# Performance work log

Hardware: AMD Instinct MI355X
Metric: run time of the kernel (lower is better)

The kernel has to match this reference:

```python
import jax, jax.numpy as jnp
import numpy as np

B = 128
N_ATOMS = 4096
NB, NA, NT = 4095, 4094, 4093
MAX_LEN = 5 * NT  # 20465, longest packed column (torsions)
EPS = 1e-8


def setup_inputs() -> dict:
    key = jax.random.key(0)
    ks = jax.random.split(key, 24)
    feats = jnp.zeros((B, MAX_LEN, 9), jnp.float32)
    # col 0: atom type ids
    atoms = jax.random.randint(ks[0], (B, N_ATOMS), 0, 6)
    # col 5: coords, flattened (N_ATOMS, 3)
    coords = jax.random.normal(ks[1], (B, N_ATOMS, 3), jnp.float32) * 5.0
    # col 6: bonds (i, j, type)
    bonds = jnp.stack([
        jax.random.randint(ks[2], (B, NB), 0, N_ATOMS),
        jax.random.randint(ks[3], (B, NB), 0, N_ATOMS),
        jax.random.randint(ks[4], (B, NB), 0, 15)], axis=-1)
    # col 7: angles (i, j, k, type)
    angles = jnp.stack([
        jax.random.randint(ks[5], (B, NA), 0, N_ATOMS),
        jax.random.randint(ks[6], (B, NA), 0, N_ATOMS),
        jax.random.randint(ks[7], (B, NA), 0, N_ATOMS),
        jax.random.randint(ks[8], (B, NA), 0, 13)], axis=-1)
    # col 8: torsions (i, j, k, l, type)
    tors = jnp.stack([
        jax.random.randint(ks[9], (B, NT), 0, N_ATOMS),
        jax.random.randint(ks[10], (B, NT), 0, N_ATOMS),
        jax.random.randint(ks[11], (B, NT), 0, N_ATOMS),
        jax.random.randint(ks[12], (B, NT), 0, N_ATOMS),
        jax.random.randint(ks[13], (B, NT), 0, 25)], axis=-1)
    feats = feats.at[:, :N_ATOMS, 0].set(atoms.astype(jnp.float32))
    feats = feats.at[:, :3 * N_ATOMS, 5].set(coords.reshape(B, -1))
    feats = feats.at[:, :3 * NB, 6].set(bonds.reshape(B, -1).astype(jnp.float32))
    feats = feats.at[:, :4 * NA, 7].set(angles.reshape(B, -1).astype(jnp.float32))
    feats = feats.at[:, :5 * NT, 8].set(tors.reshape(B, -1).astype(jnp.float32))
    lengths = jnp.tile(jnp.array(
        [[N_ATOMS, 0, 0, 0, 0, 3 * N_ATOMS, 3 * NB, 4 * NA, 5 * NT]],
        jnp.int32), (B, 1))
    bond_type = jnp.stack([jnp.ones(15), jax.random.uniform(ks[14], (15,), minval=1.0, maxval=2.0)], -1).astype(jnp.float32)
    angle_type = jnp.stack([jnp.ones(13), jax.random.uniform(ks[15], (13,), minval=1.0, maxval=3.0)], -1).astype(jnp.float32)
    tor_type = jnp.stack([jnp.ones(25), jax.random.uniform(ks[16], (25,), minval=0.0, maxval=3.14)], -1).astype(jnp.float32)
    multiplicity = jax.random.randint(ks[17], (25,), 1, 4)
    opt_pars = jax.random.uniform(ks[18], (47,), minval=0.5, maxval=1.5).astype(jnp.float32)
    return {"features": feats, "lengths": lengths, "bond_type": bond_type,
            "angle_type": angle_type, "tor_type": tor_type,
            "multiplicity": multiplicity, "opt_pars": opt_pars}


def _sample_energy(f, bond_type, angle_type, tor_type, multiplicity, opt_pars):
    coords = f[:3 * N_ATOMS, 5].reshape(-1, 3)                      # [N,3]
    bonds = f[:3 * NB, 6].astype(jnp.int32).reshape(-1, 3)          # [NB,3]
    angles = f[:4 * NA, 7].astype(jnp.int32).reshape(-1, 4)         # [NA,4]
    tors = f[:5 * NT, 8].astype(jnp.int32).reshape(-1, 5)           # [NT,5]

    # bonds: harmonic k*(r - r0)^2
    d = coords[bonds[:, 0]] - coords[bonds[:, 1]]
    r = jnp.sqrt(jnp.sum(d * d, -1) + EPS)
    pb = bond_type[bonds[:, 2]]
    e_bond = opt_pars[0] * jnp.sum(pb[:, 0] * (r - pb[:, 1]) ** 2)

    # angles: harmonic k*(theta - theta0)^2
    v1 = coords[angles[:, 0]] - coords[angles[:, 1]]
    v2 = coords[angles[:, 2]] - coords[angles[:, 1]]
    cosang = jnp.sum(v1 * v2, -1) / (
        jnp.sqrt(jnp.sum(v1 * v1, -1) + EPS) * jnp.sqrt(jnp.sum(v2 * v2, -1) + EPS))
    theta = jnp.arccos(jnp.clip(cosang, -1.0 + 1e-6, 1.0 - 1e-6))
    pa = angle_type[angles[:, 3]]
    e_ang = opt_pars[1] * jnp.sum(pa[:, 0] * (theta - pa[:, 1]) ** 2)

    # torsions: periodic k*(1 + cos(n*phi - delta))
    ci, cj, ck, cl = (coords[tors[:, m]] for m in range(4))
    b1, b2, b3 = cj - ci, ck - cj, cl - ck
    n1 = jnp.cross(b1, b2)
    n2 = jnp.cross(b2, b3)
    b2n = b2 / jnp.sqrt(jnp.sum(b2 * b2, -1, keepdims=True) + EPS)
    m1 = jnp.cross(n1, b2n)
    phi = jnp.arctan2(jnp.sum(m1 * n2, -1), jnp.sum(n1 * n2, -1))
    pt = tor_type[tors[:, 4]]
    n_mult = multiplicity[tors[:, 4]].astype(jnp.float32)
    e_tor = opt_pars[2] * jnp.sum(pt[:, 0] * (1.0 + jnp.cos(n_mult * phi - pt[:, 1])))

    return jnp.stack([e_bond, e_ang, e_tor])


def reference(features, lengths, bond_type, angle_type, tor_type, multiplicity, opt_pars):
    # lengths are uniform across batch (constants above); vmap over batch dim
    return jax.vmap(_sample_energy, in_axes=(0, None, None, None, None, None))(
        features, bond_type, angle_type, tor_type, multiplicity, opt_pars)
```

## Files before the change

### kernel.cpp

```cpp
#include <hip/hip_runtime.h>
#include <math.h>

#define BATCH   128
#define N_ATOMS 4096
#define NB      4095
#define NA      4094
#define NT      4093
#define MAX_LEN (5 * NT)
#define FSTRIDE ((size_t)MAX_LEN * 9)
#define EPSV    1e-8f
#define PARTS   6
#define THREADS 256

__global__ __launch_bounds__(THREADS) void
local_energy_kernel(const float* __restrict__ F,
                    const float* __restrict__ bond_type,
                    const float* __restrict__ angle_type,
                    const float* __restrict__ tor_type,
                    const int*   __restrict__ multiplicity,
                    const float* __restrict__ opt_pars,
                    float*       __restrict__ out)
{
    __shared__ float scx[N_ATOMS];
    __shared__ float scy[N_ATOMS];
    __shared__ float scz[N_ATOMS];
    __shared__ float sbt[30];
    __shared__ float sat[26];
    __shared__ float stt[50];
    __shared__ float smu[25];
    __shared__ float sred[12];

    const int b   = blockIdx.x;
    const int x   = b & 7;
    const int g   = b >> 3;
    const int s   = (g & 15) * 8 + x;
    const int p   = g >> 4;
    const int tid = threadIdx.x;
    const float* __restrict__ Fb = F + (size_t)s * FSTRIDE;

    if (tid < 30)                      sbt[tid]       = bond_type[tid];
    else if (tid >= 32 && tid < 58)    sat[tid - 32]  = angle_type[tid - 32];
    else if (tid >= 64 && tid < 114)   stt[tid - 64]  = tor_type[tid - 64];
    else if (tid >= 128 && tid < 153)  smu[tid - 128] = (float)multiplicity[tid - 128];

    for (int a = tid; a < N_ATOMS; a += THREADS) {
        const float* cp = Fb + 27 * a;
        float vx = cp[5];
        float vy = cp[14];
        float vz = cp[23];
        scx[a] = vx;
        scy[a] = vy;
        scz[a] = vz;
    }
    __syncthreads();

    float e_bond = 0.0f, e_ang = 0.0f, e_tor = 0.0f;

    {
        const int chunk = (NB + PARTS - 1) / PARTS;
        const int lo = p * chunk;
        const int hi = (lo + chunk < NB) ? (lo + chunk) : NB;
        for (int i = lo + tid; i < hi; i += THREADS) {
            const float* bp = Fb + 27 * i + 6;
            int a0 = (int)bp[0];
            int a1 = (int)bp[9];
            int bt = (int)bp[18];
            float dx = scx[a0] - scx[a1];
            float dy = scy[a0] - scy[a1];
            float dz = scz[a0] - scz[a1];
            float r  = sqrtf(dx*dx + dy*dy + dz*dz + EPSV);
            float k0 = sbt[bt * 2 + 0];
            float r0 = sbt[bt * 2 + 1];
            float t  = r - r0;
            e_bond += k0 * t * t;
        }
    }

    {
        const int chunk = (NA + PARTS - 1) / PARTS;
        const int lo = p * chunk;
        const int hi = (lo + chunk < NA) ? (lo + chunk) : NA;
        for (int i = lo + tid; i < hi; i += THREADS) {
            const float* ap = Fb + 36 * i + 7;
            int a0 = (int)ap[0];
            int a1 = (int)ap[9];
            int a2 = (int)ap[18];
            int at = (int)ap[27];
            float v1x = scx[a0] - scx[a1];
            float v1y = scy[a0] - scy[a1];
            float v1z = scz[a0] - scz[a1];
            float v2x = scx[a2] - scx[a1];
            float v2y = scy[a2] - scy[a1];
            float v2z = scz[a2] - scz[a1];
            float d12 = v1x*v2x + v1y*v2y + v1z*v2z;
            float n1  = sqrtf(v1x*v1x + v1y*v1y + v1z*v1z + EPSV);
            float n2  = sqrtf(v2x*v2x + v2y*v2y + v2z*v2z + EPSV);
            float cosang = d12 / (n1 * n2);
            cosang = fminf(fmaxf(cosang, -1.0f + 1e-6f), 1.0f - 1e-6f);
            float theta = acosf(cosang);
            float k0 = sat[at * 2 + 0];
            float t0 = sat[at * 2 + 1];
            float t  = theta - t0;
            e_ang += k0 * t * t;
        }
    }

    {
        const int chunk = (NT + PARTS - 1) / PARTS;
        const int lo = p * chunk;
        const int hi = (lo + chunk < NT) ? (lo + chunk) : NT;
        for (int i = lo + tid; i < hi; i += THREADS) {
            const float* tp = Fb + 45 * i + 8;
            int ai = (int)tp[0];
            int aj = (int)tp[9];
            int ak = (int)tp[18];
            int al = (int)tp[27];
            int tt = (int)tp[36];

            float cix = scx[ai], ciy = scy[ai], ciz = scz[ai];
            float cjx = scx[aj], cjy = scy[aj], cjz = scz[aj];
            float ckx = scx[ak], cky = scy[ak], ckz = scz[ak];
            float clx = scx[al], cly = scy[al], clz = scz[al];

            float b1x = cjx - cix, b1y = cjy - ciy, b1z = cjz - ciz;
            float b2x = ckx - cjx, b2y = cky - cjy, b2z = ckz - cjz;
            float b3x = clx - ckx, b3y = cly - cky, b3z = clz - ckz;

            float n1x = b1y*b2z - b1z*b2y;
            float n1y = b1z*b2x - b1x*b2z;
            float n1z = b1x*b2y - b1y*b2x;
            float n2x = b2y*b3z - b2z*b3y;
            float n2y = b2z*b3x - b2x*b3z;
            float n2z = b2x*b3y - b2y*b3x;

            float b2len = sqrtf(b2x*b2x + b2y*b2y + b2z*b2z + EPSV);
            float inv   = 1.0f / b2len;
            float bnx = b2x * inv, bny = b2y * inv, bnz = b2z * inv;

            float m1x = n1y*bnz - n1z*bny;
            float m1y = n1z*bnx - n1x*bnz;
            float m1z = n1x*bny - n1y*bnx;

            float sy = m1x*n2x + m1y*n2y + m1z*n2z;
            float sx = n1x*n2x + n1y*n2y + n1z*n2z;
            float phi = atan2f(sy, sx);

            float k0  = stt[tt * 2 + 0];
            float ph0 = stt[tt * 2 + 1];
            float nm  = smu[tt];
            e_tor += k0 * (1.0f + cosf(nm * phi - ph0));
        }
    }

    for (int off = 32; off > 0; off >>= 1) {
        e_bond += __shfl_down(e_bond, off);
        e_ang  += __shfl_down(e_ang,  off);
        e_tor  += __shfl_down(e_tor,  off);
    }
    const int wave = tid >> 6;
    const int lane = tid & 63;
    if (lane == 0) {
        sred[wave * 3 + 0] = e_bond;
        sred[wave * 3 + 1] = e_ang;
        sred[wave * 3 + 2] = e_tor;
    }
    __syncthreads();
    if (tid == 0) {
        float eb = 0.0f, ea = 0.0f, et = 0.0f;
        for (int w = 0; w < THREADS / 64; ++w) {
            eb += sred[w * 3 + 0];
            ea += sred[w * 3 + 1];
            et += sred[w * 3 + 2];
        }
        atomicAdd(&out[s * 3 + 0], opt_pars[0] * eb);
        atomicAdd(&out[s * 3 + 1], opt_pars[1] * ea);
        atomicAdd(&out[s * 3 + 2], opt_pars[2] * et);
    }
}

extern "C" void kernel_launch(void* const* d_in, const int* in_sizes, int n_in,
                              void* d_out, int out_size, void* d_ws, size_t ws_size,
                              hipStream_t stream) {
    const float* F            = (const float*)d_in[0];
    const float* bond_type    = (const float*)d_in[2];
    const float* angle_type   = (const float*)d_in[3];
    const float* tor_type     = (const float*)d_in[4];
    const int*   multiplicity = (const int*)  d_in[5];
    const float* opt_pars     = (const float*)d_in[6];
    float* out = (float*)d_out;

    hipMemsetAsync(out, 0, (size_t)out_size * sizeof(float), stream);

    dim3 grid(BATCH * PARTS);
    dim3 block(THREADS);
    local_energy_kernel<<<grid, block, 0, stream>>>(
        F, bond_type, angle_type, tor_type, multiplicity, opt_pars, out);
}
```

Measured before the change: 174.0 us.

## Stage all packed index columns into LDS with vectorized row loads, split work per term

The kernel now reads each feature row as one vectorized load covering columns 5-8 and stages coordinates and the bond, angle and torsion indices, packed as 16-bit values, into shared memory. The old version did strided scalar global loads for every interaction. Each sample gets two 1024-thread blocks, one for bonds plus angles and one for torsions, so the memset and atomics are replaced by direct stores. This risks large LDS use, low occupancy, load imbalance between the two block types, and misaligned vector loads.

```diff
diff --git a/kernel.cpp b/kernel.cpp
--- a/kernel.cpp
+++ b/kernel.cpp
@@ -1,34 +1,38 @@
 #include <hip/hip_runtime.h>
 #include <math.h>
 
-#define BATCH   128
-#define N_ATOMS 4096
-#define NB      4095
-#define NA      4094
-#define NT      4093
-#define MAX_LEN (5 * NT)
-#define FSTRIDE ((size_t)MAX_LEN * 9)
-#define EPSV    1e-8f
-#define PARTS   6
-#define THREADS 256
+#define BATCH    128
+#define N_ATOMS  4096
+#define NB       4095
+#define NA       4094
+#define NT       4093
+#define FSTRIDE  184185
+#define ROWS     20465
+#define CROWS    12288
+#define BROWS    12285
+#define AROWS    16376
+#define EPSV     1e-8f
+#define THREADS  1024
+#define WAVES    16
+#define TPR      120
 
-__global__ __launch_bounds__(THREADS) void
-local_energy_kernel(const float* __restrict__ F,
-                    const float* __restrict__ bond_type,
-                    const float* __restrict__ angle_type,
-                    const float* __restrict__ tor_type,
-                    const int*   __restrict__ multiplicity,
-                    const float* __restrict__ opt_pars,
-                    float*       __restrict__ out)
+typedef float float4a __attribute__((ext_vector_type(4), aligned(4)));
+
+__global__ __launch_bounds__(THREADS, 1) void
+local_energy_v11(const float* __restrict__ F,
+                 const float* __restrict__ bond_type,
+                 const float* __restrict__ angle_type,
+                 const float* __restrict__ tor_type,
+                 const int*   __restrict__ multiplicity,
+                 const float* __restrict__ opt_pars,
+                 float*       __restrict__ out)
 {
-    __shared__ float scx[N_ATOMS];
-    __shared__ float scy[N_ATOMS];
-    __shared__ float scz[N_ATOMS];
-    __shared__ float sbt[30];
-    __shared__ float sat[26];
-    __shared__ float stt[50];
-    __shared__ float smu[25];
-    __shared__ float sred[12];
+    __shared__ float          scc[CROWS];
+    __shared__ unsigned short sbB[BROWS + 1];
+    __shared__ unsigned short sbA[AROWS];
+    __shared__ unsigned short sbT[ROWS + 1];
+    __shared__ float sbt[30], sat[26], stt[50], smu[25];
+    __shared__ float sred[WAVES * 2];
 
     const int b   = blockIdx.x;
     const int x   = b & 7;
@@ -36,145 +40,137 @@
     const int s   = (g & 15) * 8 + x;
     const int p   = g >> 4;
     const int tid = threadIdx.x;
-    const float* __restrict__ Fb = F + (size_t)s * FSTRIDE;
+    const int w   = tid >> 6;
+    const int l   = tid & 63;
+    const size_t sbase = (size_t)s * FSTRIDE;
 
     if (tid < 30)                      sbt[tid]       = bond_type[tid];
     else if (tid >= 32 && tid < 58)    sat[tid - 32]  = angle_type[tid - 32];
     else if (tid >= 64 && tid < 114)   stt[tid - 64]  = tor_type[tid - 64];
     else if (tid >= 128 && tid < 153)  smu[tid - 128] = (float)multiplicity[tid - 128];
 
-    for (int a = tid; a < N_ATOMS; a += THREADS) {
-        const float* cp = Fb + 27 * a;
-        float vx = cp[5];
-        float vy = cp[14];
-        float vz = cp[23];
-        scx[a] = vx;
-        scy[a] = vy;
-        scz[a] = vz;
+    const int tmax = p ? 137 : 171;
+    for (int t = w; t < tmax; t += WAVES) {
+        const int R0 = TPR * t + 2 * l;
+        const int R1 = R0 + 1;
+        float4a v0, v1;
+        const bool ok0 = (R0 < ROWS);
+        const bool ok1 = (R1 < ROWS);
+        if (ok0) v0 = *(const float4a*)(F + sbase + (size_t)9 * R0 + 5);
+        if (ok1) v1 = *(const float4a*)(F + sbase + (size_t)9 * R1 + 5);
+
+        if (R1 < CROWS) {
+            float2 c2; c2.x = v0.x; c2.y = v1.x;
+            *(float2*)(scc + R0) = c2;
+        }
+        if (p) {
+            if (R1 < BROWS) {
+                unsigned pk = (unsigned)(unsigned short)(int)v0.y
+                            | ((unsigned)(unsigned short)(int)v1.y << 16);
+                *(unsigned*)(sbB + R0) = pk;
+            } else if (R0 < BROWS) {
+                sbB[R0] = (unsigned short)(int)v0.y;
+            }
+            if (R1 < AROWS) {
+                unsigned pk = (unsigned)(unsigned short)(int)v0.z
+                            | ((unsigned)(unsigned short)(int)v1.z << 16);
+                *(unsigned*)(sbA + R0) = pk;
+            }
+        } else {
+            if (ok1) {
+                unsigned pk = (unsigned)(unsigned short)(int)v0.w
+                            | ((unsigned)(unsigned short)(int)v1.w << 16);
+                *(unsigned*)(sbT + R0) = pk;
+            } else if (ok0) {
+                sbT[R0] = (unsigned short)(int)v0.w;
+            }
+        }
     }
     __syncthreads();
 
-    float e_bond = 0.0f, e_ang = 0.0f, e_tor = 0.0f;
-
-    {
-        const int chunk = (NB + PARTS - 1) / PARTS;
-        const int lo = p * chunk;
-        const int hi = (lo + chunk < NB) ? (lo + chunk) : NB;
-        for (int i = lo + tid; i < hi; i += THREADS) {
-            const float* bp = Fb + 27 * i + 6;
-            int a0 = (int)bp[0];
-            int a1 = (int)bp[9];
-            int bt = (int)bp[18];
-            float dx = scx[a0] - scx[a1];
-            float dy = scy[a0] - scy[a1];
-            float dz = scz[a0] - scz[a1];
-            float r  = sqrtf(dx*dx + dy*dy + dz*dz + EPSV);
-            float k0 = sbt[bt * 2 + 0];
-            float r0 = sbt[bt * 2 + 1];
-            float t  = r - r0;
-            e_bond += k0 * t * t;
+    float eA = 0.f, eB = 0.f;
+    if (p) {
+        for (int i = tid; i < NB; i += THREADS) {
+            const int a0 = sbB[3 * i + 0];
+            const int a1 = sbB[3 * i + 1];
+            const int bt = sbB[3 * i + 2];
+            const float dx = scc[3 * a0 + 0] - scc[3 * a1 + 0];
+            const float dy = scc[3 * a0 + 1] - scc[3 * a1 + 1];
+            const float dz = scc[3 * a0 + 2] - scc[3 * a1 + 2];
+            const float r  = sqrtf(dx * dx + dy * dy + dz * dz + EPSV);
+            const float t0 = r - sbt[bt * 2 + 1];
+            eA += sbt[bt * 2 + 0] * t0 * t0;
         }
-    }
-
-    {
-        const int chunk = (NA + PARTS - 1) / PARTS;
-        const int lo = p * chunk;
-        const int hi = (lo + chunk < NA) ? (lo + chunk) : NA;
-        for (int i = lo + tid; i < hi; i += THREADS) {
-            const float* ap = Fb + 36 * i + 7;
-            int a0 = (int)ap[0];
-            int a1 = (int)ap[9];
-            int a2 = (int)ap[18];
-            int at = (int)ap[27];
-            float v1x = scx[a0] - scx[a1];
-            float v1y = scy[a0] - scy[a1];
-            float v1z = scz[a0] - scz[a1];
-            float v2x = scx[a2] - scx[a1];
-            float v2y = scy[a2] - scy[a1];
-            float v2z = scz[a2] - scz[a1];
-            float d12 = v1x*v2x + v1y*v2y + v1z*v2z;
-            float n1  = sqrtf(v1x*v1x + v1y*v1y + v1z*v1z + EPSV);
-            float n2  = sqrtf(v2x*v2x + v2y*v2y + v2z*v2z + EPSV);
+        for (int i = tid; i < NA; i += THREADS) {
+            const int a0 = sbA[4 * i + 0];
+            const int a1 = sbA[4 * i + 1];
+            const int a2 = sbA[4 * i + 2];
+            const int at = sbA[4 * i + 3];
+            const float v1x = scc[3 * a0 + 0] - scc[3 * a1 + 0];
+            const float v1y = scc[3 * a0 + 1] - scc[3 * a1 + 1];
+            const float v1z = scc[3 * a0 + 2] - scc[3 * a1 + 2];
+            const float v2x = scc[3 * a2 + 0] - scc[3 * a1 + 0];
+            const float v2y = scc[3 * a2 + 1] - scc[3 * a1 + 1];
+            const float v2z = scc[3 * a2 + 2] - scc[3 * a1 + 2];
+            const float d12 = v1x * v2x + v1y * v2y + v1z * v2z;
+            const float n1  = sqrtf(v1x * v1x + v1y * v1y + v1z * v1z + EPSV);
+            const float n2  = sqrtf(v2x * v2x + v2y * v2y + v2z * v2z + EPSV);
             float cosang = d12 / (n1 * n2);
             cosang = fminf(fmaxf(cosang, -1.0f + 1e-6f), 1.0f - 1e-6f);
-            float theta = acosf(cosang);
-            float k0 = sat[at * 2 + 0];
-            float t0 = sat[at * 2 + 1];
-            float t  = theta - t0;
-            e_ang += k0 * t * t;
+            const float t0 = acosf(cosang) - sat[at * 2 + 1];
+            eB += sat[at * 2 + 0] * t0 * t0;
         }
-    }
-
-    {
-        const int chunk = (NT + PARTS - 1) / PARTS;
-        const int lo = p * chunk;
-        const int hi = (lo + chunk < NT) ? (lo + chunk) : NT;
-        for (int i = lo + tid; i < hi; i += THREADS) {
-            const float* tp = Fb + 45 * i + 8;
-            int ai = (int)tp[0];
-            int aj = (int)tp[9];
-            int ak = (int)tp[18];
-            int al = (int)tp[27];
-            int tt = (int)tp[36];
-
-            float cix = scx[ai], ciy = scy[ai], ciz = scz[ai];
-            float cjx = scx[aj], cjy = scy[aj], cjz = scz[aj];
-            float ckx = scx[ak], cky = scy[ak], ckz = scz[ak];
-            float clx = scx[al], cly = scy[al], clz = scz[al];
-
-            float b1x = cjx - cix, b1y = cjy - ciy, b1z = cjz - ciz;
-            float b2x = ckx - cjx, b2y = cky - cjy, b2z = ckz - cjz;
-            float b3x = clx - ckx, b3y = cly - cky, b3z = clz - ckz;
-
-            float n1x = b1y*b2z - b1z*b2y;
-            float n1y = b1z*b2x - b1x*b2z;
-            float n1z = b1x*b2y - b1y*b2x;
-            float n2x = b2y*b3z - b2z*b3y;
-            float n2y = b2z*b3x - b2x*b3z;
-            float n2z = b2x*b3y - b2y*b3x;
-
-            float b2len = sqrtf(b2x*b2x + b2y*b2y + b2z*b2z + EPSV);
-            float inv   = 1.0f / b2len;
-            float bnx = b2x * inv, bny = b2y * inv, bnz = b2z * inv;
-
-            float m1x = n1y*bnz - n1z*bny;
-            float m1y = n1z*bnx - n1x*bnz;
-            float m1z = n1x*bny - n1y*bnx;
-
-            float sy = m1x*n2x + m1y*n2y + m1z*n2z;
-            float sx = n1x*n2x + n1y*n2y + n1z*n2z;
-            float phi = atan2f(sy, sx);
-
-            float k0  = stt[tt * 2 + 0];
-            float ph0 = stt[tt * 2 + 1];
-            float nm  = smu[tt];
-            e_tor += k0 * (1.0f + cosf(nm * phi - ph0));
+    } else {
+        for (int i = tid; i < NT; i += THREADS) {
+            const int ai = sbT[5 * i + 0];
+            const int aj = sbT[5 * i + 1];
+            const int ak = sbT[5 * i + 2];
+            const int al = sbT[5 * i + 3];
+            const int tt = sbT[5 * i + 4];
+            const float b1x = scc[3*aj+0] - scc[3*ai+0];
+            const float b1y = scc[3*aj+1] - scc[3*ai+1];
+            const float b1z = scc[3*aj+2] - scc[3*ai+2];
+            const float b2x = scc[3*ak+0] - scc[3*aj+0];
+            const float b2y = scc[3*ak+1] - scc[3*aj+1];
+            const float b2z = scc[3*ak+2] - scc[3*aj+2];
+            const float b3x = scc[3*al+0] - scc[3*ak+0];
+            const float b3y = scc[3*al+1] - scc[3*ak+1];
+            const float b3z = scc[3*al+2] - scc[3*ak+2];
+            const float n1x = b1y*b2z - b1z*b2y;
+            const float n1y = b1z*b2x - b1x*b2z;
+            const float n1z = b1x*b2y - b1y*b2x;
+            const float n2x = b2y*b3z - b2z*b3y;
+            const float n2y = b2z*b3x - b2x*b3z;
+            const float n2z = b2x*b3y - b2y*b3x;
+            const float inv = 1.0f / sqrtf(b2x*b2x + b2y*b2y + b2z*b2z + EPSV);
+            const float bnx = b2x * inv, bny = b2y * inv, bnz = b2z * inv;
+            const float m1x = n1y*bnz - n1z*bny;
+            const float m1y = n1z*bnx - n1x*bnz;
+            const float m1z = n1x*bny - n1y*bnx;
+            const float phi = atan2f(m1x*n2x + m1y*n2y + m1z*n2z,
+                                     n1x*n2x + n1y*n2y + n1z*n2z);
+            eA += stt[tt * 2 + 0] * (1.0f + cosf(smu[tt] * phi - stt[tt * 2 + 1]));
         }
     }
 
     for (int off = 32; off > 0; off >>= 1) {
-        e_bond += __shfl_down(e_bond, off);
-        e_ang  += __shfl_down(e_ang,  off);
-        e_tor  += __shfl_down(e_tor,  off);
+        eA += __shfl_down(eA, off);
+        eB += __shfl_down(eB, off);
     }
-    const int wave = tid >> 6;
-    const int lane = tid & 63;
-    if (lane == 0) {
-        sred[wave * 3 + 0] = e_bond;
-        sred[wave * 3 + 1] = e_ang;
-        sred[wave * 3 + 2] = e_tor;
+    if (l == 0) {
+        sred[w * 2 + 0] = eA;
+        sred[w * 2 + 1] = eB;
     }
     __syncthreads();
     if (tid == 0) {
-        float eb = 0.0f, ea = 0.0f, et = 0.0f;
-        for (int w = 0; w < THREADS / 64; ++w) {
-            eb += sred[w * 3 + 0];
-            ea += sred[w * 3 + 1];
-            et += sred[w * 3 + 2];
+        float rA = 0.f, rB = 0.f;
+        for (int i = 0; i < WAVES; ++i) { rA += sred[i * 2]; rB += sred[i * 2 + 1]; }
+        if (p) {
+            out[s * 3 + 0] = opt_pars[0] * rA;
+            out[s * 3 + 1] = opt_pars[1] * rB;
+        } else {
+            out[s * 3 + 2] = opt_pars[2] * rA;
         }
-        atomicAdd(&out[s * 3 + 0], opt_pars[0] * eb);
-        atomicAdd(&out[s * 3 + 1], opt_pars[1] * ea);
-        atomicAdd(&out[s * 3 + 2], opt_pars[2] * et);
     }
 }
 
@@ -189,10 +185,6 @@
     const float* opt_pars     = (const float*)d_in[6];
     float* out = (float*)d_out;
 
-    hipMemsetAsync(out, 0, (size_t)out_size * sizeof(float), stream);
-
-    dim3 grid(BATCH * PARTS);
-    dim3 block(THREADS);
-    local_energy_kernel<<<grid, block, 0, stream>>>(
+    local_energy_v11<<<dim3(BATCH * 2), dim3(THREADS), 0, stream>>>(
         F, bond_type, angle_type, tor_type, multiplicity, opt_pars, out);
 }
```

Measured after the change: 155.8 us. 1.12x faster.
